# Performance work log

Measured on AMD Instinct MI355X. Metric: run time of the kernel, lower is better.

The kernel has to match this reference:

```python
import jax, jax.numpy as jnp
import numpy as np

B, S, D, H = 4, 1024, 1024, 16
HD = D // H  # 64
EPS = 1e-5

def _ln(x, g, b):
    m = jnp.mean(x, axis=-1, keepdims=True)
    v = jnp.mean(jnp.square(x - m), axis=-1, keepdims=True)
    return (x - m) * jax.lax.rsqrt(v + EPS) * g + b

def setup_inputs() -> dict:
    key = jax.random.key(0)
    ks = jax.random.split(key, 16)
    std = 0.02
    return {
        "query_tokens": jax.random.normal(ks[0], (B, S, D), jnp.float32),
        "keyvalue_tokens": jax.random.normal(ks[1], (B, S, D), jnp.float32),
        "ln_q_g": jnp.ones((D,), jnp.float32),
        "ln_q_b": jnp.zeros((D,), jnp.float32),
        "ln_kv_g": jnp.ones((D,), jnp.float32),
        "ln_kv_b": jnp.zeros((D,), jnp.float32),
        "Wq": jax.random.normal(ks[2], (2 * D, D), jnp.float32) * std,
        "Wk": jax.random.normal(ks[3], (2 * D, D), jnp.float32) * std,
        "Wv": jax.random.normal(ks[4], (2 * D, D), jnp.float32) * std,
        "Wo": jax.random.normal(ks[5], (D, 2 * D), jnp.float32) * std,
        "lambda_q1": jax.random.normal(ks[6], (HD,), jnp.float32) * 0.1,
        "lambda_k1": jax.random.normal(ks[7], (HD,), jnp.float32) * 0.1,
        "lambda_q2": jax.random.normal(ks[8], (HD,), jnp.float32) * 0.1,
        "lambda_k2": jax.random.normal(ks[9], (HD,), jnp.float32) * 0.1,
        "hn_g": jnp.ones((2 * HD,), jnp.float32),
        "hn_b": jnp.zeros((2 * HD,), jnp.float32),
        "lambda_init": jnp.float32(0.8),
        "disable_second_term": 0,
    }

def reference(query_tokens, keyvalue_tokens, ln_q_g, ln_q_b, ln_kv_g, ln_kv_b,
              Wq, Wk, Wv, Wo, lambda_q1, lambda_k1, lambda_q2, lambda_k2,
              hn_g, hn_b, lambda_init, disable_second_term):
    scale = 1.0 / np.sqrt(HD)
    q_ln = _ln(query_tokens, ln_q_g, ln_q_b)
    kv_ln = _ln(keyvalue_tokens, ln_kv_g, ln_kv_b)
    # projections: torch Linear => x @ W.T ; reshape to [B, H, S, 2*HD]
    def proj(x, W):
        y = jnp.einsum('bsd,ed->bse', x, W)
        return y.reshape(B, S, H, 2 * HD).transpose(0, 2, 1, 3)
    q = proj(q_ln, Wq)
    k = proj(kv_ln, Wk)
    v = proj(kv_ln, Wv)
    q1, q2 = q[..., :HD], q[..., HD:]
    k1, k2 = k[..., :HD], k[..., HD:]
    scores1 = jnp.einsum('bhsd,bhtd->bhst', q1, k1) * scale
    scores2 = jnp.einsum('bhsd,bhtd->bhst', q2, k2) * scale
    attn1 = jax.nn.softmax(scores1, axis=-1)
    attn2 = jax.nn.softmax(scores2, axis=-1)
    if disable_second_term:
        lam = jnp.zeros((), query_tokens.dtype)
    else:
        lam = (jnp.exp(jnp.dot(lambda_q1, lambda_k1))
               - jnp.exp(jnp.dot(lambda_q2, lambda_k2)) + lambda_init)
    out = jnp.einsum('bhst,bhtd->bhsd', attn1 - lam * attn2, v)  # [B,H,S,2HD]
    out = _ln(out, hn_g, hn_b) * (1.0 - lambda_init)
    out = out.transpose(0, 2, 1, 3).reshape(B, S, 2 * D)
    out = jnp.einsum('bse,de->bsd', out, Wo)
    return query_tokens + out
```

## Files before the change

kernel.cpp:

```cpp
#include <hip/hip_runtime.h>
#include <stdint.h>

#define B_  4
#define S_  1024
#define D_  1024
#define H_  16
#define HD_ 64
#define E_  2048
#define C2_ 128

typedef __attribute__((ext_vector_type(8))) short          bf16x8;
typedef __attribute__((ext_vector_type(8))) unsigned short u16x8;
typedef __attribute__((ext_vector_type(4))) unsigned short u16x4;
typedef __attribute__((ext_vector_type(4))) float          f32x4;

#define QSCALE 0.18033688f

__device__ __forceinline__ unsigned short f2bf(float f) {
  union { float f; unsigned int u; } v; v.f = f;
  unsigned int r = v.u + 0x7fffu + ((v.u >> 16) & 1u);
  return (unsigned short)(r >> 16);
}

__device__ __forceinline__ unsigned int cvtpk_bf16(float lo, float hi) {
  unsigned int r;
  asm("v_cvt_pk_bf16_f32 %0, %1, %2" : "=v"(r) : "v"(lo), "v"(hi));
  return r;
}

__device__ __forceinline__ float red16_sum(float x) {
  x += __int_as_float(__builtin_amdgcn_mov_dpp(__float_as_int(x), 0xB1, 0xF, 0xF, false));
  x += __int_as_float(__builtin_amdgcn_mov_dpp(__float_as_int(x), 0x4E, 0xF, 0xF, false));
  x += __int_as_float(__builtin_amdgcn_mov_dpp(__float_as_int(x), 0x141, 0xF, 0xF, false));
  x += __int_as_float(__builtin_amdgcn_mov_dpp(__float_as_int(x), 0x140, 0xF, 0xF, false));
  return x;
}

typedef const __attribute__((address_space(1))) unsigned int* gas1_t;
typedef __attribute__((address_space(3))) unsigned int* las3_t;
__device__ __forceinline__ void gload16(const void* g, void* s) {
  __builtin_amdgcn_global_load_lds((gas1_t)g, (las3_t)s, 16, 0, 0);
}

__global__ __launch_bounds__(256) void ln_cast_k(const float* __restrict__ x,
                                                 const float* __restrict__ g,
                                                 const float* __restrict__ bb,
                                                 unsigned short* __restrict__ out) {
  int row = blockIdx.x;
  int tid = threadIdx.x;
  const float* xr = x + (size_t)row * D_;
  float4 xv = *(const float4*)(xr + tid * 4);
  float s  = xv.x + xv.y + xv.z + xv.w;
  float sq = xv.x * xv.x + xv.y * xv.y + xv.z * xv.z + xv.w * xv.w;
#pragma unroll
  for (int m = 32; m; m >>= 1) { s += __shfl_xor(s, m, 64); sq += __shfl_xor(sq, m, 64); }
  __shared__ float ps[4], pq[4];
  int w = tid >> 6, l = tid & 63;
  if (l == 0) { ps[w] = s; pq[w] = sq; }
  __syncthreads();
  s  = ps[0] + ps[1] + ps[2] + ps[3];
  sq = pq[0] + pq[1] + pq[2] + pq[3];
  float mean = s * (1.f / D_);
  float var  = sq * (1.f / D_) - mean * mean;
  float rstd = rsqrtf(var + 1e-5f);
  float4 gv = *(const float4*)(g + tid * 4);
  float4 bv = *(const float4*)(bb + tid * 4);
  u16x4 o;
  o.x = f2bf((xv.x - mean) * rstd * gv.x + bv.x);
  o.y = f2bf((xv.y - mean) * rstd * gv.y + bv.y);
  o.z = f2bf((xv.z - mean) * rstd * gv.z + bv.z);
  o.w = f2bf((xv.w - mean) * rstd * gv.w + bv.w);
  *(u16x4*)(out + (size_t)row * D_ + tid * 4) = o;
}

__global__ __launch_bounds__(256) void cast_k(const float* __restrict__ in,
                                              unsigned short* __restrict__ out, int n4) {
  int i = blockIdx.x * 256 + threadIdx.x;
  if (i < n4) {
    float4 v = *(const float4*)(in + (size_t)i * 4);
    u16x4 o; o.x = f2bf(v.x); o.y = f2bf(v.y); o.z = f2bf(v.z); o.w = f2bf(v.w);
    *(u16x4*)(out + (size_t)i * 4) = o;
  }
}

__global__ __launch_bounds__(256) void gemm_proj_k(
    const unsigned short* __restrict__ qln, const unsigned short* __restrict__ kvln,
    const unsigned short* __restrict__ Wq,  const unsigned short* __restrict__ Wk,
    const unsigned short* __restrict__ Wv,
    unsigned short* __restrict__ qb, unsigned short* __restrict__ kb,
    unsigned short* __restrict__ vtb) {
  const int K = D_;
  int which = blockIdx.z;
  const unsigned short* A = (which == 0) ? qln : kvln;
  const unsigned short* W = (which == 0) ? Wq : (which == 1 ? Wk : Wv);
  unsigned short* O = (which == 0) ? qb : (which == 1 ? kb : vtb);
  int m0 = blockIdx.y * 128, n0 = blockIdx.x * 128;
  __shared__ __align__(16) char psm[128 * 272];
  char* lsA = psm;
  char* lsB = psm + 16384;
  int tid = threadIdx.x, l = tid & 63, w = tid >> 6;
  int wm = (w >> 1) * 64, wn = (w & 1) * 64;
  f32x4 acc[4][4] = {};
  for (int kt = 0; kt < K; kt += 64) {
    __syncthreads();
#pragma unroll
    for (int i = 0; i < 4; i++) {
      int rbase = (i * 4 + w) * 8;
      int row = rbase + (l >> 3), c8 = l & 7;
      int sc = (c8 ^ (row & 7)) * 8;
      gload16(A + (size_t)(m0 + row) * K + kt + sc, lsA + rbase * 128);
      gload16(W + (size_t)(n0 + row) * K + kt + sc, lsB + rbase * 128);
    }
    __syncthreads();
#pragma unroll
    for (int kk = 0; kk < 2; kk++) {
      bf16x8 af[4], bfr[4];
      int koff = kk * 64 + (l >> 4) * 16;
#pragma unroll
      for (int mf = 0; mf < 4; mf++) {
        int row = wm + mf * 16 + (l & 15);
        af[mf] = *(const bf16x8*)(lsA + row * 128 + (koff ^ ((row & 7) << 4)));
      }
#pragma unroll
      for (int nf = 0; nf < 4; nf++) {
        int row = wn + nf * 16 + (l & 15);
        bfr[nf] = *(const bf16x8*)(lsB + row * 128 + (koff ^ ((row & 7) << 4)));
      }
#pragma unroll
      for (int mf = 0; mf < 4; mf++)
#pragma unroll
        for (int nf = 0; nf < 4; nf++)
          acc[mf][nf] = __builtin_amdgcn_mfma_f32_16x16x32_bf16(af[mf], bfr[nf], acc[mf][nf], 0, 0, 0);
    }
  }
  if (which < 2) {
    float sc = (which == 0) ? QSCALE : 1.0f;
#pragma unroll
    for (int mf = 0; mf < 4; mf++)
#pragma unroll
      for (int nf = 0; nf < 4; nf++)
#pragma unroll
        for (int r = 0; r < 4; r++) {
          int gm = m0 + wm + mf * 16 + (l >> 4) * 4 + r;
          int gn = n0 + wn + nf * 16 + (l & 15);
          int b = gm >> 10, s = gm & 1023;
          int h = gn >> 7,  c = gn & 127;
          O[((size_t)((b * H_ + h) * S_ + s)) * C2_ + c] = f2bf(acc[mf][nf][r] * sc);
        }
  } else {
    __syncthreads();
#pragma unroll
    for (int mf = 0; mf < 4; mf++)
#pragma unroll
      for (int nf = 0; nf < 4; nf++) {
        int crow = wn + nf * 16 + (l & 15);
        int sloc = wm + mf * 16 + (l >> 4) * 4;
        u16x4 pk4;
        pk4.x = f2bf(acc[mf][nf][0]); pk4.y = f2bf(acc[mf][nf][1]);
        pk4.z = f2bf(acc[mf][nf][2]); pk4.w = f2bf(acc[mf][nf][3]);
        *(u16x4*)(psm + (size_t)crow * 272 + sloc * 2) = pk4;
      }
    __syncthreads();
    int b = m0 >> 10, sbase = m0 & 1023;
#pragma unroll
    for (int i = 0; i < 8; i++) {
      int u2 = i * 256 + tid;
      int row = u2 >> 4, c16 = u2 & 15;
      u16x8 vv = *(const u16x8*)(psm + (size_t)row * 272 + c16 * 16);
      int gn = n0 + row, h = gn >> 7, cfeat = gn & 127;
      *(u16x8*)(O + ((size_t)((b * H_ + h) * C2_ + cfeat)) * S_ + sbase + c16 * 8) = vv;
    }
  }
}

__global__ __launch_bounds__(256) void gemm_out_k(
    const unsigned short* __restrict__ A, const unsigned short* __restrict__ W,
    const float* __restrict__ resid, float* __restrict__ out) {
  const int K = E_;
  int m0 = blockIdx.y * 128, n0 = blockIdx.x * 128;
  __shared__ __align__(16) char psm2[32768];
  char* lsA = psm2;
  char* lsB = psm2 + 16384;
  int tid = threadIdx.x, l = tid & 63, w = tid >> 6;
  int wm = (w >> 1) * 64, wn = (w & 1) * 64;
  f32x4 acc[4][4] = {};
  for (int kt = 0; kt < K; kt += 64) {
    __syncthreads();
#pragma unroll
    for (int i = 0; i < 4; i++) {
      int rbase = (i * 4 + w) * 8;
      int row = rbase + (l >> 3), c8 = l & 7;
      int sc = (c8 ^ (row & 7)) * 8;
      gload16(A + (size_t)(m0 + row) * K + kt + sc, lsA + rbase * 128);
      gload16(W + (size_t)(n0 + row) * K + kt + sc, lsB + rbase * 128);
    }
    __syncthreads();
#pragma unroll
    for (int kk = 0; kk < 2; kk++) {
      bf16x8 af[4], bfr[4];
      int koff = kk * 64 + (l >> 4) * 16;
#pragma unroll
      for (int mf = 0; mf < 4; mf++) {
        int row = wm + mf * 16 + (l & 15);
        af[mf] = *(const bf16x8*)(lsA + row * 128 + (koff ^ ((row & 7) << 4)));
      }
#pragma unroll
      for (int nf = 0; nf < 4; nf++) {
        int row = wn + nf * 16 + (l & 15);
        bfr[nf] = *(const bf16x8*)(lsB + row * 128 + (koff ^ ((row & 7) << 4)));
      }
#pragma unroll
      for (int mf = 0; mf < 4; mf++)
#pragma unroll
        for (int nf = 0; nf < 4; nf++)
          acc[mf][nf] = __builtin_amdgcn_mfma_f32_16x16x32_bf16(af[mf], bfr[nf], acc[mf][nf], 0, 0, 0);
    }
  }
#pragma unroll
  for (int mf = 0; mf < 4; mf++)
#pragma unroll
    for (int nf = 0; nf < 4; nf++)
#pragma unroll
      for (int r = 0; r < 4; r++) {
        int gm = m0 + wm + mf * 16 + (l >> 4) * 4 + r;
        int gn = n0 + wn + nf * 16 + (l & 15);
        size_t idx = (size_t)gm * D_ + gn;
        out[idx] = acc[mf][nf][r] + resid[idx];
      }
}

__global__ __launch_bounds__(256) void attn_k(
    const unsigned short* __restrict__ q, const unsigned short* __restrict__ k,
    const unsigned short* __restrict__ vt,
    const float* __restrict__ lq1, const float* __restrict__ lk1,
    const float* __restrict__ lq2, const float* __restrict__ lk2,
    const float* __restrict__ hng, const float* __restrict__ hnb,
    const float* __restrict__ lambda_init, const int* __restrict__ dis2,
    unsigned short* __restrict__ out) {
  int bh = blockIdx.x;
  int qt = blockIdx.y;
  int tid = threadIdx.x, ln = tid & 63, w = tid >> 6;
  int g = ln >> 4, c = ln & 15;
  bool godd = (g & 1);
  __shared__ unsigned short lsK[2][64 * 128];
  __shared__ unsigned short lsVt[2][128 * 64];
  __shared__ float s_lam, s_osc;

  if (tid < 64) {
    float a = lq1[ln] * lk1[ln];
    float cc = lq2[ln] * lk2[ln];
#pragma unroll
    for (int m = 32; m; m >>= 1) { a += __shfl_xor(a, m, 64); cc += __shfl_xor(cc, m, 64); }
    if (ln == 0) {
      float li = lambda_init[0];
      float lam = __expf(a) - __expf(cc) + li;
      if (dis2[0] != 0) lam = 0.f;
      s_lam = lam;
      s_osc = 1.f - li;
    }
  }

  const unsigned short* kbh = k + (size_t)bh * S_ * C2_;
  const unsigned short* vbh = vt + (size_t)bh * C2_ * S_;

  int qrow = qt * 64 + w * 16 + c;
  const unsigned short* qrp = q + ((size_t)bh * S_ + qrow) * C2_;
  bf16x8 qf[2][2];
#pragma unroll
  for (int t = 0; t < 2; t++)
#pragma unroll
    for (int kk = 0; kk < 2; kk++)
      qf[t][kk] = *(const bf16x8*)(qrp + t * 64 + kk * 32 + g * 8);

  f32x4 lones[2] = {};
  f32x4 o[2][8] = {};
  bf16x8 onesf;
#pragma unroll
  for (int j = 0; j < 8; j++) onesf[j] = (short)0x3F80;

#define STAGE_KV(buf, t0s)                                                            \
  {                                                                                   \
    const unsigned short* kbase = kbh + (size_t)(t0s) * C2_;                          \
    _Pragma("unroll")                                                                 \
    for (int i = 0; i < 4; i++) {                                                     \
      int rb = w * 16 + i * 4;                                                        \
      int row = rb + (ln >> 4), c16 = ln & 15;                                        \
      gload16(kbase + row * C2_ + ((c16 ^ (row & 7)) * 8),                            \
              (char*)&lsK[buf][0] + rb * 256);                                        \
    }                                                                                 \
    const unsigned short* vbase = vbh + (t0s);                                        \
    _Pragma("unroll")                                                                 \
    for (int i = 0; i < 4; i++) {                                                     \
      int rb = w * 32 + i * 8;                                                        \
      int row = rb + (ln >> 3), c8 = ln & 7;                                          \
      gload16(vbase + (size_t)row * S_ + ((c8 ^ (row & 7)) * 8),                      \
              (char*)&lsVt[buf][0] + rb * 128);                                       \
    }                                                                                 \
  }

  STAGE_KV(0, 0);
  __syncthreads();

  for (int it = 0; it < S_ / 64; ++it) {
    int cur = it & 1;
    if (it + 1 < S_ / 64) STAGE_KV(cur ^ 1, (it + 1) * 64);

    unsigned int paw[2][2][4];

#pragma unroll
    for (int term = 0; term < 2; term++) {
      f32x4 sf[4] = {};
      __builtin_amdgcn_s_setprio(1);
#pragma unroll
      for (int kk = 0; kk < 2; kk++) {
#pragma unroll
        for (int nf = 0; nf < 4; nf++) {
          int kfrow = nf * 16 + c;
          bf16x8 kf = *(const bf16x8*)((char*)&lsK[cur][0] + kfrow * 256 +
                        ((term * 128 + kk * 64 + g * 16) ^ ((kfrow & 7) << 4)));
          sf[nf] = __builtin_amdgcn_mfma_f32_16x16x32_bf16(kf, qf[term][kk], sf[nf], 0, 0, 0);
        }
      }
      __builtin_amdgcn_s_setprio(0);
#pragma unroll
      for (int nf = 0; nf < 4; nf++)
#pragma unroll
        for (int r = 0; r < 4; r++)
          sf[nf][r] = exp2f(sf[nf][r]);
#pragma unroll
      for (int kk = 0; kk < 2; kk++) {
        unsigned int X0 = cvtpk_bf16(sf[2 * kk][0], sf[2 * kk][1]);
        unsigned int X1 = cvtpk_bf16(sf[2 * kk][2], sf[2 * kk][3]);
        unsigned int Y0 = cvtpk_bf16(sf[2 * kk + 1][0], sf[2 * kk + 1][1]);
        unsigned int Y1 = cvtpk_bf16(sf[2 * kk + 1][2], sf[2 * kk + 1][3]);
        asm("v_permlane32_swap_b32 %0, %1" : "+v"(X0), "+v"(Y0));
        asm("v_permlane32_swap_b32 %0, %1" : "+v"(X1), "+v"(Y1));
        {
          unsigned int t0w = __shfl_xor((int)Y0, 16), u0 = __shfl_xor((int)X0, 16);
          unsigned int t1w = __shfl_xor((int)Y1, 16), u1 = __shfl_xor((int)X1, 16);
          unsigned int nX0 = godd ? t0w : X0, nY0 = godd ? Y0 : u0;
          unsigned int nX1 = godd ? t1w : X1, nY1 = godd ? Y1 : u1;
          paw[term][kk][0] = nX0; paw[term][kk][1] = nX1;
          paw[term][kk][2] = nY0; paw[term][kk][3] = nY1;
        }
      }
    }

#pragma unroll
    for (int kk = 0; kk < 2; kk++) {
      union { unsigned int u[4]; bf16x8 v; } pa0, pa1;
#pragma unroll
      for (int j = 0; j < 4; j++) { pa0.u[j] = paw[0][kk][j]; pa1.u[j] = paw[1][kk][j]; }
      __builtin_amdgcn_s_setprio(1);
      lones[0] = __builtin_amdgcn_mfma_f32_16x16x32_bf16(pa0.v, onesf, lones[0], 0, 0, 0);
      lones[1] = __builtin_amdgcn_mfma_f32_16x16x32_bf16(pa1.v, onesf, lones[1], 0, 0, 0);
#pragma unroll
      for (int nf2 = 0; nf2 < 8; nf2++) {
        int vrow = nf2 * 16 + c;
        bf16x8 vf = *(const bf16x8*)((char*)&lsVt[cur][0] + vrow * 128 +
                      ((kk * 64 + g * 16) ^ ((vrow & 7) << 4)));
        o[0][nf2] = __builtin_amdgcn_mfma_f32_16x16x32_bf16(pa0.v, vf, o[0][nf2], 0, 0, 0);
        o[1][nf2] = __builtin_amdgcn_mfma_f32_16x16x32_bf16(pa1.v, vf, o[1][nf2], 0, 0, 0);
      }
      __builtin_amdgcn_s_setprio(0);
    }
    __syncthreads();
  }

  float lam = s_lam, osc = s_osc;
  int b = bh >> 4, h = bh & 15;
#pragma unroll
  for (int r = 0; r < 4; r++) {
    float inv1 = 1.f / lones[0][r];
    float inv2 = lam / lones[1][r];
    float vals[8];
    float sum = 0.f, sq = 0.f;
#pragma unroll
    for (int nf2 = 0; nf2 < 8; nf2++) {
      float vv = o[0][nf2][r] * inv1 - o[1][nf2][r] * inv2;
      vals[nf2] = vv;
      sum += vv; sq += vv * vv;
    }
    sum = red16_sum(sum);
    sq  = red16_sum(sq);
    float mean = sum * (1.f / 128.f);
    float var  = sq * (1.f / 128.f) - mean * mean;
    float rstd = rsqrtf(var + 1e-5f);
    int srow = qt * 64 + w * 16 + g * 4 + r;
    unsigned short* orow = out + ((size_t)(b * S_ + srow)) * E_ + h * C2_;
#pragma unroll
    for (int nf2 = 0; nf2 < 8; nf2++) {
      int feat = nf2 * 16 + c;
      float y = (vals[nf2] - mean) * rstd * hng[feat] + hnb[feat];
      orow[feat] = f2bf(y * osc);
    }
  }
}

extern "C" void kernel_launch(void* const* d_in, const int* in_sizes, int n_in,
                              void* d_out, int out_size, void* d_ws, size_t ws_size,
                              hipStream_t stream) {
  const float* qtok = (const float*)d_in[0];
  const float* kvtok = (const float*)d_in[1];
  const float* lnqg = (const float*)d_in[2];
  const float* lnqb = (const float*)d_in[3];
  const float* lnkg = (const float*)d_in[4];
  const float* lnkb = (const float*)d_in[5];
  const float* Wq = (const float*)d_in[6];
  const float* Wk = (const float*)d_in[7];
  const float* Wv = (const float*)d_in[8];
  const float* Wo = (const float*)d_in[9];
  const float* lq1 = (const float*)d_in[10];
  const float* lk1 = (const float*)d_in[11];
  const float* lq2 = (const float*)d_in[12];
  const float* lk2 = (const float*)d_in[13];
  const float* hng = (const float*)d_in[14];
  const float* hnb = (const float*)d_in[15];
  const float* lami = (const float*)d_in[16];
  const int*   dis2 = (const int*)d_in[17];
  float* outp = (float*)d_out;

  char* ws = (char*)d_ws;
  const size_t MB = 1024 * 1024;
  unsigned short* qln    = (unsigned short*)(ws + 0);
  unsigned short* kvln   = (unsigned short*)(ws + 8 * MB);
  unsigned short* attn_o = (unsigned short*)(ws + 0);
  unsigned short* Wqb = (unsigned short*)(ws + 16 * MB);
  unsigned short* Wkb = (unsigned short*)(ws + 20 * MB);
  unsigned short* Wvb = (unsigned short*)(ws + 24 * MB);
  unsigned short* Wob = (unsigned short*)(ws + 28 * MB);
  unsigned short* qb  = (unsigned short*)(ws + 32 * MB);
  unsigned short* kb  = (unsigned short*)(ws + 48 * MB);
  unsigned short* vtb = (unsigned short*)(ws + 64 * MB);

  ln_cast_k<<<dim3(4096), dim3(256), 0, stream>>>(qtok, lnqg, lnqb, qln);
  ln_cast_k<<<dim3(4096), dim3(256), 0, stream>>>(kvtok, lnkg, lnkb, kvln);
  cast_k<<<dim3(2048), dim3(256), 0, stream>>>(Wq, Wqb, 512 * 1024);
  cast_k<<<dim3(2048), dim3(256), 0, stream>>>(Wk, Wkb, 512 * 1024);
  cast_k<<<dim3(2048), dim3(256), 0, stream>>>(Wv, Wvb, 512 * 1024);
  cast_k<<<dim3(2048), dim3(256), 0, stream>>>(Wo, Wob, 512 * 1024);
  gemm_proj_k<<<dim3(16, 32, 3), dim3(256), 0, stream>>>(qln, kvln, Wqb, Wkb, Wvb, qb, kb, vtb);
  attn_k<<<dim3(64, 16), dim3(256), 0, stream>>>(qb, kb, vtb, lq1, lk1, lq2, lk2,
                                                 hng, hnb, lami, dis2, attn_o);
  gemm_out_k<<<dim3(8, 32), dim3(256), 0, stream>>>(attn_o, Wob, qtok, outp);
}
```

Before: 217.7 us.

## Process two 16-row query sub-tiles per wave in attention kernel

Each wave now handles 32 query rows (two 16-row sub-tiles) instead of 16, so every K and V fragment read from LDS feeds twice as many MFMAs. The grid's query-tile dimension is halved to match, and launch bounds now request two blocks per CU. This is meant to cut LDS traffic and K/V staging per query row. The cost is a doubled accumulator footprint and higher register pressure, which the launch-bounds hint may turn into spills, plus fewer blocks in the grid.

New measurement: 222.8 us. 2.4% more time.

```diff
diff --git a/kernel.cpp b/kernel.cpp
--- a/kernel.cpp
+++ b/kernel.cpp
@@ -229,7 +229,7 @@
       }
 }
 
-__global__ __launch_bounds__(256) void attn_k(
+__global__ __launch_bounds__(256, 2) void attn_k(
     const unsigned short* __restrict__ q, const unsigned short* __restrict__ k,
     const unsigned short* __restrict__ vt,
     const float* __restrict__ lq1, const float* __restrict__ lk1,
@@ -263,17 +263,20 @@
   const unsigned short* kbh = k + (size_t)bh * S_ * C2_;
   const unsigned short* vbh = vt + (size_t)bh * C2_ * S_;
 
-  int qrow = qt * 64 + w * 16 + c;
-  const unsigned short* qrp = q + ((size_t)bh * S_ + qrow) * C2_;
-  bf16x8 qf[2][2];
-#pragma unroll
-  for (int t = 0; t < 2; t++)
-#pragma unroll
-    for (int kk = 0; kk < 2; kk++)
-      qf[t][kk] = *(const bf16x8*)(qrp + t * 64 + kk * 32 + g * 8);
-
-  f32x4 lones[2] = {};
-  f32x4 o[2][8] = {};
+  bf16x8 qf[2][2][2];
+#pragma unroll
+  for (int sub = 0; sub < 2; sub++) {
+    int qrow = qt * 128 + w * 32 + sub * 16 + c;
+    const unsigned short* qrp = q + ((size_t)bh * S_ + qrow) * C2_;
+#pragma unroll
+    for (int t = 0; t < 2; t++)
+#pragma unroll
+      for (int kk = 0; kk < 2; kk++)
+        qf[sub][t][kk] = *(const bf16x8*)(qrp + t * 64 + kk * 32 + g * 8);
+  }
+
+  f32x4 lones[2][2] = {};
+  f32x4 o[2][2][8] = {};
   bf16x8 onesf;
 #pragma unroll
   for (int j = 0; j < 8; j++) onesf[j] = (short)0x3F80;
@@ -305,11 +308,11 @@
     int cur = it & 1;
     if (it + 1 < S_ / 64) STAGE_KV(cur ^ 1, (it + 1) * 64);
 
-    unsigned int paw[2][2][4];
+    unsigned int paw[2][2][2][4];
 
 #pragma unroll
     for (int term = 0; term < 2; term++) {
-      f32x4 sf[4] = {};
+      f32x4 sf[2][4] = {};
       __builtin_amdgcn_s_setprio(1);
 #pragma unroll
       for (int kk = 0; kk < 2; kk++) {
@@ -318,49 +321,61 @@
           int kfrow = nf * 16 + c;
           bf16x8 kf = *(const bf16x8*)((char*)&lsK[cur][0] + kfrow * 256 +
                         ((term * 128 + kk * 64 + g * 16) ^ ((kfrow & 7) << 4)));
-          sf[nf] = __builtin_amdgcn_mfma_f32_16x16x32_bf16(kf, qf[term][kk], sf[nf], 0, 0, 0);
+          sf[0][nf] = __builtin_amdgcn_mfma_f32_16x16x32_bf16(kf, qf[0][term][kk], sf[0][nf], 0, 0, 0);
+          sf[1][nf] = __builtin_amdgcn_mfma_f32_16x16x32_bf16(kf, qf[1][term][kk], sf[1][nf], 0, 0, 0);
         }
       }
       __builtin_amdgcn_s_setprio(0);
 #pragma unroll
-      for (int nf = 0; nf < 4; nf++)
-#pragma unroll
-        for (int r = 0; r < 4; r++)
-          sf[nf][r] = exp2f(sf[nf][r]);
-#pragma unroll
-      for (int kk = 0; kk < 2; kk++) {
-        unsigned int X0 = cvtpk_bf16(sf[2 * kk][0], sf[2 * kk][1]);
-        unsigned int X1 = cvtpk_bf16(sf[2 * kk][2], sf[2 * kk][3]);
-        unsigned int Y0 = cvtpk_bf16(sf[2 * kk + 1][0], sf[2 * kk + 1][1]);
-        unsigned int Y1 = cvtpk_bf16(sf[2 * kk + 1][2], sf[2 * kk + 1][3]);
-        asm("v_permlane32_swap_b32 %0, %1" : "+v"(X0), "+v"(Y0));
-        asm("v_permlane32_swap_b32 %0, %1" : "+v"(X1), "+v"(Y1));
-        {
+      for (int sub = 0; sub < 2; sub++) {
+#pragma unroll
+        for (int nf = 0; nf < 4; nf++)
+#pragma unroll
+          for (int r = 0; r < 4; r++)
+            sf[sub][nf][r] = exp2f(sf[sub][nf][r]);
+#pragma unroll
+        for (int kk = 0; kk < 2; kk++) {
+          unsigned int X0 = cvtpk_bf16(sf[sub][2 * kk][0], sf[sub][2 * kk][1]);
+          unsigned int X1 = cvtpk_bf16(sf[sub][2 * kk][2], sf[sub][2 * kk][3]);
+          unsigned int Y0 = cvtpk_bf16(sf[sub][2 * kk + 1][0], sf[sub][2 * kk + 1][1]);
+          unsigned int Y1 = cvtpk_bf16(sf[sub][2 * kk + 1][2], sf[sub][2 * kk + 1][3]);
+          asm("v_permlane32_swap_b32 %0, %1" : "+v"(X0), "+v"(Y0));
+          asm("v_permlane32_swap_b32 %0, %1" : "+v"(X1), "+v"(Y1));
           unsigned int t0w = __shfl_xor((int)Y0, 16), u0 = __shfl_xor((int)X0, 16);
           unsigned int t1w = __shfl_xor((int)Y1, 16), u1 = __shfl_xor((int)X1, 16);
-          unsigned int nX0 = godd ? t0w : X0, nY0 = godd ? Y0 : u0;
-          unsigned int nX1 = godd ? t1w : X1, nY1 = godd ? Y1 : u1;
-          paw[term][kk][0] = nX0; paw[term][kk][1] = nX1;
-          paw[term][kk][2] = nY0; paw[term][kk][3] = nY1;
+          paw[sub][term][kk][0] = godd ? t0w : X0;
+          paw[sub][term][kk][1] = godd ? t1w : X1;
+          paw[sub][term][kk][2] = godd ? Y0 : u0;
+          paw[sub][term][kk][3] = godd ? Y1 : u1;
         }
       }
     }
 
 #pragma unroll
     for (int kk = 0; kk < 2; kk++) {
-      union { unsigned int u[4]; bf16x8 v; } pa0, pa1;
-#pragma unroll
-      for (int j = 0; j < 4; j++) { pa0.u[j] = paw[0][kk][j]; pa1.u[j] = paw[1][kk][j]; }
+      union { unsigned int u[4]; bf16x8 v; } pa[2][2];
+#pragma unroll
+      for (int sub = 0; sub < 2; sub++)
+#pragma unroll
+        for (int term = 0; term < 2; term++)
+#pragma unroll
+          for (int j = 0; j < 4; j++) pa[sub][term].u[j] = paw[sub][term][kk][j];
       __builtin_amdgcn_s_setprio(1);
-      lones[0] = __builtin_amdgcn_mfma_f32_16x16x32_bf16(pa0.v, onesf, lones[0], 0, 0, 0);
-      lones[1] = __builtin_amdgcn_mfma_f32_16x16x32_bf16(pa1.v, onesf, lones[1], 0, 0, 0);
+#pragma unroll
+      for (int sub = 0; sub < 2; sub++) {
+        lones[sub][0] = __builtin_amdgcn_mfma_f32_16x16x32_bf16(pa[sub][0].v, onesf, lones[sub][0], 0, 0, 0);
+        lones[sub][1] = __builtin_amdgcn_mfma_f32_16x16x32_bf16(pa[sub][1].v, onesf, lones[sub][1], 0, 0, 0);
+      }
 #pragma unroll
       for (int nf2 = 0; nf2 < 8; nf2++) {
         int vrow = nf2 * 16 + c;
         bf16x8 vf = *(const bf16x8*)((char*)&lsVt[cur][0] + vrow * 128 +
                       ((kk * 64 + g * 16) ^ ((vrow & 7) << 4)));
-        o[0][nf2] = __builtin_amdgcn_mfma_f32_16x16x32_bf16(pa0.v, vf, o[0][nf2], 0, 0, 0);
-        o[1][nf2] = __builtin_amdgcn_mfma_f32_16x16x32_bf16(pa1.v, vf, o[1][nf2], 0, 0, 0);
+#pragma unroll
+        for (int sub = 0; sub < 2; sub++) {
+          o[sub][0][nf2] = __builtin_amdgcn_mfma_f32_16x16x32_bf16(pa[sub][0].v, vf, o[sub][0][nf2], 0, 0, 0);
+          o[sub][1][nf2] = __builtin_amdgcn_mfma_f32_16x16x32_bf16(pa[sub][1].v, vf, o[sub][1][nf2], 0, 0, 0);
+        }
       }
       __builtin_amdgcn_s_setprio(0);
     }
@@ -370,31 +385,33 @@
   float lam = s_lam, osc = s_osc;
   int b = bh >> 4, h = bh & 15;
 #pragma unroll
-  for (int r = 0; r < 4; r++) {
-    float inv1 = 1.f / lones[0][r];
-    float inv2 = lam / lones[1][r];
-    float vals[8];
-    float sum = 0.f, sq = 0.f;
-#pragma unroll
-    for (int nf2 = 0; nf2 < 8; nf2++) {
-      float vv = o[0][nf2][r] * inv1 - o[1][nf2][r] * inv2;
-      vals[nf2] = vv;
-      sum += vv; sq += vv * vv;
-    }
-    sum = red16_sum(sum);
-    sq  = red16_sum(sq);
-    float mean = sum * (1.f / 128.f);
-    float var  = sq * (1.f / 128.f) - mean * mean;
-    float rstd = rsqrtf(var + 1e-5f);
-    int srow = qt * 64 + w * 16 + g * 4 + r;
-    unsigned short* orow = out + ((size_t)(b * S_ + srow)) * E_ + h * C2_;
-#pragma unroll
-    for (int nf2 = 0; nf2 < 8; nf2++) {
-      int feat = nf2 * 16 + c;
-      float y = (vals[nf2] - mean) * rstd * hng[feat] + hnb[feat];
-      orow[feat] = f2bf(y * osc);
-    }
-  }
+  for (int sub = 0; sub < 2; sub++)
+#pragma unroll
+    for (int r = 0; r < 4; r++) {
+      float inv1 = 1.f / lones[sub][0][r];
+      float inv2 = lam / lones[sub][1][r];
+      float vals[8];
+      float sum = 0.f, sq = 0.f;
+#pragma unroll
+      for (int nf2 = 0; nf2 < 8; nf2++) {
+        float vv = o[sub][0][nf2][r] * inv1 - o[sub][1][nf2][r] * inv2;
+        vals[nf2] = vv;
+        sum += vv; sq += vv * vv;
+      }
+      sum = red16_sum(sum);
+      sq  = red16_sum(sq);
+      float mean = sum * (1.f / 128.f);
+      float var  = sq * (1.f / 128.f) - mean * mean;
+      float rstd = rsqrtf(var + 1e-5f);
+      int srow = qt * 128 + w * 32 + sub * 16 + g * 4 + r;
+      unsigned short* orow = out + ((size_t)(b * S_ + srow)) * E_ + h * C2_;
+#pragma unroll
+      for (int nf2 = 0; nf2 < 8; nf2++) {
+        int feat = nf2 * 16 + c;
+        float y = (vals[nf2] - mean) * rstd * hng[feat] + hnb[feat];
+        orow[feat] = f2bf(y * osc);
+      }
+    }
 }
 
 extern "C" void kernel_launch(void* const* d_in, const int* in_sizes, int n_in,
@@ -440,7 +457,7 @@
   cast_k<<<dim3(2048), dim3(256), 0, stream>>>(Wv, Wvb, 512 * 1024);
   cast_k<<<dim3(2048), dim3(256), 0, stream>>>(Wo, Wob, 512 * 1024);
   gemm_proj_k<<<dim3(16, 32, 3), dim3(256), 0, stream>>>(qln, kvln, Wqb, Wkb, Wvb, qb, kb, vtb);
-  attn_k<<<dim3(64, 16), dim3(256), 0, stream>>>(qb, kb, vtb, lq1, lk1, lq2, lk2,
-                                                 hng, hnb, lami, dis2, attn_o);
+  attn_k<<<dim3(64, 8), dim3(256), 0, stream>>>(qb, kb, vtb, lq1, lk1, lq2, lk2,
+                                                hng, hnb, lami, dis2, attn_o);
   gemm_out_k<<<dim3(8, 32), dim3(256), 0, stream>>>(attn_o, Wob, qtok, outp);
 }
```

## Read K/V fragments directly from global memory instead of LDS staging

Applied to the files above, without the earlier changes.

The attention kernel drops its double-buffered LDS staging of K and V^T tiles and the per-iteration __syncthreads. Each lane now loads its MFMA fragments straight from global memory (relying on L2/L1 for reuse across the 4 waves), and launch bounds request 4 blocks per CU. This removes LDS traffic and barrier stalls and frees LDS for higher occupancy, but each wave now issues redundant global loads for K/V with no explicit prefetch. Load latency is then exposed directly in front of the MFMAs.

Result: slower. 418.7 us (+92.3%).

```diff
diff --git a/kernel.cpp b/kernel.cpp
--- a/kernel.cpp
+++ b/kernel.cpp
@@ -229,7 +229,7 @@
       }
 }
 
-__global__ __launch_bounds__(256) void attn_k(
+__global__ __launch_bounds__(256, 4) void attn_k(
     const unsigned short* __restrict__ q, const unsigned short* __restrict__ k,
     const unsigned short* __restrict__ vt,
     const float* __restrict__ lq1, const float* __restrict__ lk1,
@@ -242,8 +242,6 @@
   int tid = threadIdx.x, ln = tid & 63, w = tid >> 6;
   int g = ln >> 4, c = ln & 15;
   bool godd = (g & 1);
-  __shared__ unsigned short lsK[2][64 * 128];
-  __shared__ unsigned short lsVt[2][128 * 64];
   __shared__ float s_lam, s_osc;
 
   if (tid < 64) {
@@ -278,33 +276,10 @@
 #pragma unroll
   for (int j = 0; j < 8; j++) onesf[j] = (short)0x3F80;
 
-#define STAGE_KV(buf, t0s)                                                            \
-  {                                                                                   \
-    const unsigned short* kbase = kbh + (size_t)(t0s) * C2_;                          \
-    _Pragma("unroll")                                                                 \
-    for (int i = 0; i < 4; i++) {                                                     \
-      int rb = w * 16 + i * 4;                                                        \
-      int row = rb + (ln >> 4), c16 = ln & 15;                                        \
-      gload16(kbase + row * C2_ + ((c16 ^ (row & 7)) * 8),                            \
-              (char*)&lsK[buf][0] + rb * 256);                                        \
-    }                                                                                 \
-    const unsigned short* vbase = vbh + (t0s);                                        \
-    _Pragma("unroll")                                                                 \
-    for (int i = 0; i < 4; i++) {                                                     \
-      int rb = w * 32 + i * 8;                                                        \
-      int row = rb + (ln >> 3), c8 = ln & 7;                                          \
-      gload16(vbase + (size_t)row * S_ + ((c8 ^ (row & 7)) * 8),                      \
-              (char*)&lsVt[buf][0] + rb * 128);                                       \
-    }                                                                                 \
-  }
-
-  STAGE_KV(0, 0);
-  __syncthreads();
-
-  for (int it = 0; it < S_ / 64; ++it) {
-    int cur = it & 1;
-    if (it + 1 < S_ / 64) STAGE_KV(cur ^ 1, (it + 1) * 64);
-
+  const unsigned short* kLane = kbh + (size_t)c * C2_ + g * 8;
+  const unsigned short* vLane = vbh + (size_t)c * S_ + g * 8;
+
+  for (int t0 = 0; t0 < S_; t0 += 64) {
     unsigned int paw[2][2][4];
 
 #pragma unroll
@@ -315,9 +290,7 @@
       for (int kk = 0; kk < 2; kk++) {
 #pragma unroll
         for (int nf = 0; nf < 4; nf++) {
-          int kfrow = nf * 16 + c;
-          bf16x8 kf = *(const bf16x8*)((char*)&lsK[cur][0] + kfrow * 256 +
-                        ((term * 128 + kk * 64 + g * 16) ^ ((kfrow & 7) << 4)));
+          bf16x8 kf = *(const bf16x8*)(kLane + (size_t)(t0 + nf * 16) * C2_ + term * 64 + kk * 32);
           sf[nf] = __builtin_amdgcn_mfma_f32_16x16x32_bf16(kf, qf[term][kk], sf[nf], 0, 0, 0);
         }
       }
@@ -335,14 +308,12 @@
         unsigned int Y1 = cvtpk_bf16(sf[2 * kk + 1][2], sf[2 * kk + 1][3]);
         asm("v_permlane32_swap_b32 %0, %1" : "+v"(X0), "+v"(Y0));
         asm("v_permlane32_swap_b32 %0, %1" : "+v"(X1), "+v"(Y1));
-        {
-          unsigned int t0w = __shfl_xor((int)Y0, 16), u0 = __shfl_xor((int)X0, 16);
-          unsigned int t1w = __shfl_xor((int)Y1, 16), u1 = __shfl_xor((int)X1, 16);
-          unsigned int nX0 = godd ? t0w : X0, nY0 = godd ? Y0 : u0;
-          unsigned int nX1 = godd ? t1w : X1, nY1 = godd ? Y1 : u1;
-          paw[term][kk][0] = nX0; paw[term][kk][1] = nX1;
-          paw[term][kk][2] = nY0; paw[term][kk][3] = nY1;
-        }
+        unsigned int t0w = __shfl_xor((int)Y0, 16), u0 = __shfl_xor((int)X0, 16);
+        unsigned int t1w = __shfl_xor((int)Y1, 16), u1 = __shfl_xor((int)X1, 16);
+        paw[term][kk][0] = godd ? t0w : X0;
+        paw[term][kk][1] = godd ? t1w : X1;
+        paw[term][kk][2] = godd ? Y0 : u0;
+        paw[term][kk][3] = godd ? Y1 : u1;
       }
     }
 
@@ -356,9 +327,7 @@
       lones[1] = __builtin_amdgcn_mfma_f32_16x16x32_bf16(pa1.v, onesf, lones[1], 0, 0, 0);
 #pragma unroll
       for (int nf2 = 0; nf2 < 8; nf2++) {
-        int vrow = nf2 * 16 + c;
-        bf16x8 vf = *(const bf16x8*)((char*)&lsVt[cur][0] + vrow * 128 +
-                      ((kk * 64 + g * 16) ^ ((vrow & 7) << 4)));
+        bf16x8 vf = *(const bf16x8*)(vLane + (size_t)(nf2 * 16) * S_ + t0 + kk * 32);
         o[0][nf2] = __builtin_amdgcn_mfma_f32_16x16x32_bf16(pa0.v, vf, o[0][nf2], 0, 0, 0);
         o[1][nf2] = __builtin_amdgcn_mfma_f32_16x16x32_bf16(pa1.v, vf, o[1][nf2], 0, 0, 0);
       }
```
